# Kernel optimization log

Measured on AMD Instinct MI355X. Metric: run time of the kernel, lower is better.

## Reference

```python
import jax, jax.numpy as jnp
import numpy as np

N_NODES = 100000
N_EDGES = 1600000
IN_CH = 512
MID_CH = 64   # hard-coded mid_layer_channel in the module
OUT_CH = 40


def setup_inputs() -> dict:
    key = jax.random.key(0)
    k0, k1, k2, k3 = jax.random.split(key, 4)
    node_feature = jax.random.normal(k0, (N_NODES, IN_CH), dtype=jnp.float32)
    # edge index [2, E]: row 0 = src, row 1 = dst
    adj_list = jax.random.randint(k1, (2, N_EDGES), 0, N_NODES, dtype=jnp.int32)
    # GCNConv parameters (Glorot-ish scale)
    W1 = jax.random.normal(k2, (IN_CH, MID_CH), dtype=jnp.float32) * (1.0 / np.sqrt(IN_CH))
    b1 = jnp.zeros((MID_CH,), dtype=jnp.float32)
    W2 = jax.random.normal(k3, (MID_CH, OUT_CH), dtype=jnp.float32) * (1.0 / np.sqrt(MID_CH))
    b2 = jnp.zeros((OUT_CH,), dtype=jnp.float32)
    return {"node_feature": node_feature, "adj_list": adj_list,
            "W1": W1, "b1": b1, "W2": W2, "b2": b2}


def _gcn_conv(x, W, b, src, dst, deg_inv_sqrt, n_nodes):
    # Standard GCNConv: D^{-1/2} (A + I) D^{-1/2} (x W) + b
    h = x @ W                                             # [N, F_out]
    norm = deg_inv_sqrt[src] * deg_inv_sqrt[dst]          # [E]
    agg = jax.ops.segment_sum(h[src] * norm[:, None], dst, num_segments=n_nodes)
    agg = agg + h * (deg_inv_sqrt * deg_inv_sqrt)[:, None]  # self-loop term
    return agg + b


def reference(node_feature, adj_list, W1, b1, W2, b2):
    n = node_feature.shape[0]
    src, dst = adj_list[0], adj_list[1]
    # degree with self-loops (in-degree at dst + 1)
    deg = jax.ops.segment_sum(jnp.ones_like(dst, dtype=node_feature.dtype), dst,
                              num_segments=n) + 1.0
    deg_inv_sqrt = jax.lax.rsqrt(deg)
    h = jax.nn.elu(_gcn_conv(node_feature, W1, b1, src, dst, deg_inv_sqrt, n))
    out = _gcn_conv(h, W2, b2, src, dst, deg_inv_sqrt, n)
    return jax.nn.log_softmax(out, axis=1)
```

## Files before the change

### kernel.cpp

```cpp
#include <hip/hip_runtime.h>
#include <hip/hip_bf16.h>
#include <math.h>

#define IN_CH 512
#define MID_CH 64
#define OUT_CH 40

typedef __attribute__((ext_vector_type(8))) short short8;
typedef __attribute__((ext_vector_type(4))) float f32x4;
typedef __attribute__((ext_vector_type(2))) float f32x2;

static __device__ __forceinline__ unsigned short f2bf(float f) {
    unsigned int u = __float_as_uint(f);
    u += 0x7fffu + ((u >> 16) & 1u);
    return (unsigned short)(u >> 16);
}

__global__ void k_count(const int* __restrict__ dst, int* __restrict__ cnt, int E) {
    int pb = blockIdx.x & 7;
    int ch = blockIdx.x >> 3;
    int nch = gridDim.x >> 3;
    int ech = (E + nch - 1) / nch;
    int e0 = ch * ech;
    int e1 = e0 + ech; if (e1 > E) e1 = E;
    for (int e = e0 + threadIdx.x; e < e1; e += blockDim.x) {
        int d = dst[e];
        if ((d & 7) == pb) atomicAdd(&cnt[d], 1);
    }
}

__global__ void k_scanA(const int* __restrict__ cnt, int* __restrict__ rowptr,
                        int* __restrict__ bsum, float* __restrict__ dis, int N) {
    __shared__ int wsum[16];
    int i = blockIdx.x * 1024 + threadIdx.x;
    int lane = threadIdx.x & 63, wv = threadIdx.x >> 6;
    int v = (i < N) ? cnt[i] : 0;
    if (i < N) dis[i] = rsqrtf((float)v + 1.0f);
    int x = (v + 3) & ~3;
    #pragma unroll
    for (int off = 1; off < 64; off <<= 1) {
        int t = __shfl_up(x, off);
        if (lane >= off) x += t;
    }
    if (lane == 63) wsum[wv] = x;
    __syncthreads();
    if (wv == 0 && lane < 16) {
        int own = wsum[lane];
        int y = own;
        #pragma unroll
        for (int off = 1; off < 16; off <<= 1) {
            int t = __shfl_up(y, off);
            if (lane >= off) y += t;
        }
        wsum[lane] = y - own;
        if (lane == 15) bsum[blockIdx.x] = y;
    }
    __syncthreads();
    if (i < N) rowptr[i + 1] = x + wsum[wv];
}

__global__ void k_scanB(int* __restrict__ bsum, int nb) {
    __shared__ int tmp[2];
    int lane = threadIdx.x & 63, wv = threadIdx.x >> 6;
    int v = (threadIdx.x < nb) ? bsum[threadIdx.x] : 0;
    int x = v;
    #pragma unroll
    for (int off = 1; off < 64; off <<= 1) {
        int t = __shfl_up(x, off);
        if (lane >= off) x += t;
    }
    if (lane == 63) tmp[wv] = x;
    __syncthreads();
    int add = (wv == 1) ? tmp[0] : 0;
    if (threadIdx.x < nb) bsum[threadIdx.x] = x - v + add;
}

__global__ void k_scanC(int* __restrict__ rowptr, int* __restrict__ cur,
                        const int* __restrict__ bsum, int N) {
    int i = blockIdx.x * 1024 + threadIdx.x;
    if (i < N) {
        int v = rowptr[i + 1] + bsum[blockIdx.x];
        rowptr[i + 1] = v;
        cur[i + 1] = v;
    }
    if (i == 0) { rowptr[0] = 0; cur[0] = 0; }
}

__global__ void k_padfill(int* __restrict__ esrc, int dummy_off, int total) {
    int i = blockIdx.x * blockDim.x + threadIdx.x;
    if (i < total) esrc[i] = dummy_off;
}

__global__ void k_fill(const int* __restrict__ src, const int* __restrict__ dst,
                       int* __restrict__ cur, int* __restrict__ esrc, int E) {
    int pb = blockIdx.x & 7;
    int ch = blockIdx.x >> 3;
    int nch = gridDim.x >> 3;
    int ech = (E + nch - 1) / nch;
    int e0 = ch * ech;
    int e1 = e0 + ech; if (e1 > E) e1 = E;
    #pragma unroll 4
    for (int e = e0 + (int)threadIdx.x; e < e1; e += blockDim.x) {
        int d = dst[e];
        if ((d & 7) == pb) {
            int p = atomicAdd(&cur[d], 1);
            esrc[p] = src[e] << 6;
        }
    }
}

__global__ void k_prepw(const float* __restrict__ W1, unsigned short* __restrict__ w1f) {
    int f = blockIdx.x * 256 + threadIdx.x;
    int k = f >> 6, c = f & 63;
    w1f[(((k >> 3) * 64) + c) * 8 + (k & 7)] = f2bf(W1[f]);
}

__launch_bounds__(256, 6)
__global__ void k_gemm1(const float* __restrict__ X, const unsigned short* __restrict__ w1f,
                        const float* __restrict__ dis, unsigned char* __restrict__ h1q,
                        int N) {
    int wave = threadIdx.x >> 6, lane = threadIdx.x & 63;
    int rbase = blockIdx.x * 64 + wave * 16;
    int g = lane >> 4;
    int arow = rbase + (lane & 15);
    if (arow > N - 1) arow = N - 1;
    const float* xp = X + (size_t)arow * IN_CH + g * 8;
    const short8* wb = (const short8*)w1f;

    f32x4 acc[4];
    #pragma unroll
    for (int i = 0; i < 4; ++i) acc[i] = (f32x4){0.f, 0.f, 0.f, 0.f};

    float4 bx0[2], bx1[2];
    {
        const float4* p0 = (const float4*)(xp);
        const float4* p1 = (const float4*)(xp + 32);
        bx0[0] = p0[0]; bx1[0] = p0[1];
        bx0[1] = p1[0]; bx1[1] = p1[1];
    }

    #pragma unroll
    for (int ks = 0; ks < 16; ++ks) {
        float4 x0 = bx0[ks & 1], x1 = bx1[ks & 1];
        if (ks < 14) {
            const float4* p = (const float4*)(xp + (ks + 2) * 32);
            bx0[ks & 1] = p[0]; bx1[ks & 1] = p[1];
        }
        short8 a;
        a[0] = (short)f2bf(x0.x); a[1] = (short)f2bf(x0.y);
        a[2] = (short)f2bf(x0.z); a[3] = (short)f2bf(x0.w);
        a[4] = (short)f2bf(x1.x); a[5] = (short)f2bf(x1.y);
        a[6] = (short)f2bf(x1.z); a[7] = (short)f2bf(x1.w);

        int cibase = (ks * 4 + g) * 64 + (lane & 15);
        #pragma unroll
        for (int ct = 0; ct < 4; ++ct) {
            short8 b = wb[cibase + ct * 16];
            acc[ct] = __builtin_amdgcn_mfma_f32_16x16x32_bf16(a, b, acc[ct], 0, 0, 0);
        }
    }

    int colb = lane & 15;
    int rquad = rbase + (lane >> 4) * 4;
    #pragma unroll
    for (int ct = 0; ct < 4; ++ct) {
        #pragma unroll
        for (int r = 0; r < 4; ++r) {
            int row = rquad + r;
            if (row < N) {
                float v = acc[ct][r] * dis[row];
                unsigned q = __builtin_amdgcn_cvt_pk_fp8_f32(v, v, 0, false);
                h1q[(size_t)row * 64 + ct * 16 + colb] = (unsigned char)q;
            }
        }
    }
}

#define AGG_UNPACK8(Q)                                              \
    {                                                               \
        f32x2 lo_ = __builtin_amdgcn_cvt_pk_f32_fp8((Q), false);    \
        f32x2 hi_ = __builtin_amdgcn_cvt_pk_f32_fp8((Q), true);     \
        acc[0] += lo_[0]; acc[1] += lo_[1];                         \
        acc[2] += hi_[0]; acc[3] += hi_[1];                         \
    }

__launch_bounds__(256)
__global__ void k_agg1(const unsigned char* __restrict__ hq, const float* __restrict__ dis,
                       const int* __restrict__ rowptr, const int* __restrict__ esrc,
                       const float* __restrict__ b1, unsigned char* __restrict__ h2q,
                       int N) {
    int wv = threadIdx.x >> 6, lane = threadIdx.x & 63;
    int n = blockIdx.x * 4 + wv;
    if (n >= N) return;
    int g = lane >> 4, cg = lane & 15;
    int beg = rowptr[n], end = rowptr[n + 1];
    unsigned cgoff = (unsigned)(cg * 4);
    const char* hb = (const char*)hq;

    f32x4 acc = (f32x4){0.f, 0.f, 0.f, 0.f};
    for (int cbeg = beg; cbeg < end; cbeg += 64) {
        int m = end - cbeg; if (m > 64) m = 64;
        int soff = esrc[cbeg + lane];
        int k4n = m >> 2;
        int k4 = 0;
        for (; k4 + 4 <= k4n; k4 += 4) {
            int o0 = __shfl(soff, (k4 + 0) * 4 + g);
            int o1 = __shfl(soff, (k4 + 1) * 4 + g);
            int o2 = __shfl(soff, (k4 + 2) * 4 + g);
            int o3 = __shfl(soff, (k4 + 3) * 4 + g);
            unsigned q0 = *(const unsigned*)(hb + ((unsigned)o0 + cgoff));
            unsigned q1 = *(const unsigned*)(hb + ((unsigned)o1 + cgoff));
            unsigned q2 = *(const unsigned*)(hb + ((unsigned)o2 + cgoff));
            unsigned q3 = *(const unsigned*)(hb + ((unsigned)o3 + cgoff));
            AGG_UNPACK8(q0) AGG_UNPACK8(q1) AGG_UNPACK8(q2) AGG_UNPACK8(q3)
        }
        for (; k4 < k4n; ++k4) {
            int o = __shfl(soff, k4 * 4 + g);
            unsigned q = *(const unsigned*)(hb + ((unsigned)o + cgoff));
            AGG_UNPACK8(q)
        }
    }
    #pragma unroll
    for (int off = 32; off >= 16; off >>= 1) {
        acc[0] += __shfl_xor(acc[0], off);
        acc[1] += __shfl_xor(acc[1], off);
        acc[2] += __shfl_xor(acc[2], off);
        acc[3] += __shfl_xor(acc[3], off);
    }
    if (g == 0) {
        float dn = dis[n];
        unsigned qs = *(const unsigned*)(hb + ((unsigned)(n * 64) + cgoff));
        f32x2 slo = __builtin_amdgcn_cvt_pk_f32_fp8(qs, false);
        f32x2 shi = __builtin_amdgcn_cvt_pk_f32_fp8(qs, true);
        float4 b4 = *(const float4*)(b1 + cg * 4);
        float v0 = dn * (acc[0] + slo[0]) + b4.x;
        float v1 = dn * (acc[1] + slo[1]) + b4.y;
        float v2 = dn * (acc[2] + shi[0]) + b4.z;
        float v3 = dn * (acc[3] + shi[1]) + b4.w;
        v0 = v0 > 0.f ? v0 : expm1f(v0);
        v1 = v1 > 0.f ? v1 : expm1f(v1);
        v2 = v2 > 0.f ? v2 : expm1f(v2);
        v3 = v3 > 0.f ? v3 : expm1f(v3);
        unsigned w = __builtin_amdgcn_cvt_pk_fp8_f32(dn * v0, dn * v1, 0, false);
        w = __builtin_amdgcn_cvt_pk_fp8_f32(dn * v2, dn * v3, w, true);
        *(unsigned*)(h2q + (size_t)n * 64 + cg * 4) = w;
    }
}

__launch_bounds__(256)
__global__ void k_agg2(const unsigned char* __restrict__ hq, const float* __restrict__ dis,
                       const int* __restrict__ rowptr, const int* __restrict__ esrc,
                       const float* __restrict__ W2, const float* __restrict__ b2,
                       float* __restrict__ out, int N) {
    __shared__ float w2l[MID_CH * OUT_CH];
    __shared__ float vl[4 * MID_CH];
    for (int f = threadIdx.x; f < MID_CH * OUT_CH; f += 256) w2l[f] = W2[f];
    __syncthreads();

    int wv = threadIdx.x >> 6, lane = threadIdx.x & 63;
    int n = blockIdx.x * 4 + wv;
    if (n >= N) return;
    int g = lane >> 4, cg = lane & 15;
    int beg = rowptr[n], end = rowptr[n + 1];
    unsigned cgoff = (unsigned)(cg * 4);
    const char* hb = (const char*)hq;

    f32x4 acc = (f32x4){0.f, 0.f, 0.f, 0.f};
    for (int cbeg = beg; cbeg < end; cbeg += 64) {
        int m = end - cbeg; if (m > 64) m = 64;
        int soff = esrc[cbeg + lane];
        int k4n = m >> 2;
        int k4 = 0;
        for (; k4 + 4 <= k4n; k4 += 4) {
            int o0 = __shfl(soff, (k4 + 0) * 4 + g);
            int o1 = __shfl(soff, (k4 + 1) * 4 + g);
            int o2 = __shfl(soff, (k4 + 2) * 4 + g);
            int o3 = __shfl(soff, (k4 + 3) * 4 + g);
            unsigned q0 = *(const unsigned*)(hb + ((unsigned)o0 + cgoff));
            unsigned q1 = *(const unsigned*)(hb + ((unsigned)o1 + cgoff));
            unsigned q2 = *(const unsigned*)(hb + ((unsigned)o2 + cgoff));
            unsigned q3 = *(const unsigned*)(hb + ((unsigned)o3 + cgoff));
            AGG_UNPACK8(q0) AGG_UNPACK8(q1) AGG_UNPACK8(q2) AGG_UNPACK8(q3)
        }
        for (; k4 < k4n; ++k4) {
            int o = __shfl(soff, k4 * 4 + g);
            unsigned q = *(const unsigned*)(hb + ((unsigned)o + cgoff));
            AGG_UNPACK8(q)
        }
    }
    #pragma unroll
    for (int off = 32; off >= 16; off >>= 1) {
        acc[0] += __shfl_xor(acc[0], off);
        acc[1] += __shfl_xor(acc[1], off);
        acc[2] += __shfl_xor(acc[2], off);
        acc[3] += __shfl_xor(acc[3], off);
    }
    if (g == 0) {
        float dn = dis[n];
        unsigned qs = *(const unsigned*)(hb + ((unsigned)(n * 64) + cgoff));
        f32x2 slo = __builtin_amdgcn_cvt_pk_f32_fp8(qs, false);
        f32x2 shi = __builtin_amdgcn_cvt_pk_f32_fp8(qs, true);
        float4 v;
        v.x = dn * (acc[0] + slo[0]);
        v.y = dn * (acc[1] + slo[1]);
        v.z = dn * (acc[2] + shi[0]);
        v.w = dn * (acc[3] + shi[1]);
        *(float4*)&vl[wv * 64 + cg * 4] = v;
    }

    float o = (lane < OUT_CH) ? b2[lane] : 0.f;
    const float* vrow = &vl[wv * 64];
    #pragma unroll 8
    for (int c = 0; c < MID_CH; ++c)
        o += vrow[c] * w2l[c * OUT_CH + lane];

    float mx = (lane < OUT_CH) ? o : -1e30f;
    #pragma unroll
    for (int off = 32; off > 0; off >>= 1) mx = fmaxf(mx, __shfl_xor(mx, off));
    float e = (lane < OUT_CH) ? expf(o - mx) : 0.f;
    float ssum = e;
    #pragma unroll
    for (int off = 32; off > 0; off >>= 1) ssum += __shfl_xor(ssum, off);
    if (lane < OUT_CH)
        out[(size_t)n * OUT_CH + lane] = o - mx - logf(ssum);
}

extern "C" void kernel_launch(void* const* d_in, const int* in_sizes, int n_in,
                              void* d_out, int out_size, void* d_ws, size_t ws_size,
                              hipStream_t stream) {
    const float* X  = (const float*)d_in[0];
    const int* adj  = (const int*)d_in[1];
    const float* W1 = (const float*)d_in[2];
    const float* b1 = (const float*)d_in[3];
    const float* W2 = (const float*)d_in[4];
    const float* b2 = (const float*)d_in[5];
    float* out = (float*)d_out;

    int N = in_sizes[0] / IN_CH;
    int E = in_sizes[1] / 2;
    const int* srcp = adj;
    const int* dstp = adj + E;
    int nchunk = (N + 1023) / 1024;
    int epad_max = E + 3 * N + 128;

    char* ws = (char*)d_ws;
    size_t off = 0;
    int*   cnt    = (int*)(ws + off);  off += (size_t)N * sizeof(int);
    int*   cur    = (int*)(ws + off);  off += ((size_t)N + 8) * sizeof(int);
    float* dis    = (float*)(ws + off); off += (size_t)N * sizeof(float);
    int*   rowptr = (int*)(ws + off);  off += ((size_t)N + 8) * sizeof(int);
    int*   bsum   = (int*)(ws + off);  off += 128 * sizeof(int);
    int*   esrc   = (int*)(ws + off);  off += (size_t)epad_max * sizeof(int);
    unsigned short* w1f = (unsigned short*)(ws + off); off += (size_t)IN_CH * MID_CH * sizeof(unsigned short);
    unsigned char* h1q = (unsigned char*)(ws + off); off += (size_t)(N + 4) * MID_CH;
    unsigned char* h2q = (unsigned char*)(ws + off); off += (size_t)(N + 4) * MID_CH;

    hipMemsetAsync(cnt, 0, (size_t)N * sizeof(int), stream);
    k_prepw<<<(IN_CH * MID_CH + 255) / 256, 256, 0, stream>>>(W1, w1f);
    k_count<<<512, 256, 0, stream>>>(dstp, cnt, E);
    k_scanA<<<nchunk, 1024, 0, stream>>>(cnt, rowptr, bsum, dis, N);
    k_scanB<<<1, 128, 0, stream>>>(bsum, nchunk);
    k_scanC<<<nchunk, 1024, 0, stream>>>(rowptr, cur, bsum, N);
    k_padfill<<<(epad_max + 255) / 256, 256, 0, stream>>>(esrc, N << 6, epad_max);
    hipMemsetAsync(h1q + (size_t)N * 64, 0, 64, stream);
    hipMemsetAsync(h2q + (size_t)N * 64, 0, 64, stream);

    k_fill<<<1024, 256, 0, stream>>>(srcp, dstp, cur, esrc, E);
    k_gemm1<<<(N + 63) / 64, 256, 0, stream>>>(X, w1f, dis, h1q, N);
    k_agg1<<<(N + 3) / 4, 256, 0, stream>>>(h1q, dis, rowptr, esrc, b1, h2q, N);
    k_agg2<<<(N + 3) / 4, 256, 0, stream>>>(h2q, dis, rowptr, esrc, W2, b2, out, N);
}
```

Measured before the change: 336.9 us.

## Split fp8 feature tables into 32-channel halves to shrink gather working set

Splits the layer-1 and layer-2 fp8 feature tables into two 32-byte-per-node halves and runs each aggregation twice, one pass per half. Each gather pass then reads from a 3.2MB table that fits better in cache. Edge lists are padded to multiples of 8 so each wave processes 8 edges per step. Layer 2 accumulates partial W2 products in an fp32 buffer between passes. The count kernel is also simplified to one atomic per edge. The cost is twice the edge-index traffic and launches, plus an extra partial-output round trip.

```diff
diff --git a/kernel.cpp b/kernel.cpp
--- a/kernel.cpp
+++ b/kernel.cpp
@@ -17,16 +17,8 @@
 }
 
 __global__ void k_count(const int* __restrict__ dst, int* __restrict__ cnt, int E) {
-    int pb = blockIdx.x & 7;
-    int ch = blockIdx.x >> 3;
-    int nch = gridDim.x >> 3;
-    int ech = (E + nch - 1) / nch;
-    int e0 = ch * ech;
-    int e1 = e0 + ech; if (e1 > E) e1 = E;
-    for (int e = e0 + threadIdx.x; e < e1; e += blockDim.x) {
-        int d = dst[e];
-        if ((d & 7) == pb) atomicAdd(&cnt[d], 1);
-    }
+    int i = blockIdx.x * blockDim.x + threadIdx.x;
+    if (i < E) atomicAdd(&cnt[dst[i]], 1);
 }
 
 __global__ void k_scanA(const int* __restrict__ cnt, int* __restrict__ rowptr,
@@ -36,7 +28,7 @@
     int lane = threadIdx.x & 63, wv = threadIdx.x >> 6;
     int v = (i < N) ? cnt[i] : 0;
     if (i < N) dis[i] = rsqrtf((float)v + 1.0f);
-    int x = (v + 3) & ~3;
+    int x = (v + 7) & ~7;
     #pragma unroll
     for (int off = 1; off < 64; off <<= 1) {
         int t = __shfl_up(x, off);
@@ -104,7 +96,7 @@
         int d = dst[e];
         if ((d & 7) == pb) {
             int p = atomicAdd(&cur[d], 1);
-            esrc[p] = src[e] << 6;
+            esrc[p] = src[e] << 5;
         }
     }
 }
@@ -117,7 +109,8 @@
 
 __launch_bounds__(256, 6)
 __global__ void k_gemm1(const float* __restrict__ X, const unsigned short* __restrict__ w1f,
-                        const float* __restrict__ dis, unsigned char* __restrict__ h1q,
+                        const float* __restrict__ dis,
+                        unsigned char* __restrict__ h1A, unsigned char* __restrict__ h1B,
                         int N) {
     int wave = threadIdx.x >> 6, lane = threadIdx.x & 63;
     int rbase = blockIdx.x * 64 + wave * 16;
@@ -164,13 +157,15 @@
     int rquad = rbase + (lane >> 4) * 4;
     #pragma unroll
     for (int ct = 0; ct < 4; ++ct) {
+        unsigned char* tbl = (ct < 2) ? h1A : h1B;
+        int coloff = (ct & 1) * 16 + colb;
         #pragma unroll
         for (int r = 0; r < 4; ++r) {
             int row = rquad + r;
             if (row < N) {
                 float v = acc[ct][r] * dis[row];
                 unsigned q = __builtin_amdgcn_cvt_pk_fp8_f32(v, v, 0, false);
-                h1q[(size_t)row * 64 + ct * 16 + colb] = (unsigned char)q;
+                tbl[(size_t)row * 32 + coloff] = (unsigned char)q;
             }
         }
     }
@@ -184,55 +179,55 @@
         acc[2] += hi_[0]; acc[3] += hi_[1];                         \
     }
 
+#define GATHER_CORE(HB)                                                 \
+    f32x4 acc = (f32x4){0.f, 0.f, 0.f, 0.f};                            \
+    for (int cbeg = beg; cbeg < end; cbeg += 64) {                      \
+        int m = end - cbeg; if (m > 64) m = 64;      \
+        int soff = esrc[cbeg + lane];                                   \
+        int k8n = m >> 3;                                               \
+        int k8 = 0;                                                     \
+        for (; k8 + 2 <= k8n; k8 += 2) {                                \
+            int o0 = __shfl(soff, (k8 + 0) * 8 + g);                    \
+            int o1 = __shfl(soff, (k8 + 1) * 8 + g);                    \
+            unsigned q0 = *(const unsigned*)((HB) + ((unsigned)o0 + cgoff)); \
+            unsigned q1 = *(const unsigned*)((HB) + ((unsigned)o1 + cgoff)); \
+            AGG_UNPACK8(q0) AGG_UNPACK8(q1)                             \
+        }                                                               \
+        for (; k8 < k8n; ++k8) {                                        \
+            int o = __shfl(soff, k8 * 8 + g);                           \
+            unsigned q = *(const unsigned*)((HB) + ((unsigned)o + cgoff)); \
+            AGG_UNPACK8(q)                                              \
+        }                                                               \
+    }                                                                   \
+    _Pragma("unroll")                                                   \
+    for (int off = 32; off >= 8; off >>= 1) {                           \
+        acc[0] += __shfl_xor(acc[0], off);                              \
+        acc[1] += __shfl_xor(acc[1], off);                              \
+        acc[2] += __shfl_xor(acc[2], off);                              \
+        acc[3] += __shfl_xor(acc[3], off);                              \
+    }
+
 __launch_bounds__(256)
 __global__ void k_agg1(const unsigned char* __restrict__ hq, const float* __restrict__ dis,
                        const int* __restrict__ rowptr, const int* __restrict__ esrc,
-                       const float* __restrict__ b1, unsigned char* __restrict__ h2q,
+                       const float* __restrict__ bias, unsigned char* __restrict__ hdst,
                        int N) {
     int wv = threadIdx.x >> 6, lane = threadIdx.x & 63;
     int n = blockIdx.x * 4 + wv;
     if (n >= N) return;
-    int g = lane >> 4, cg = lane & 15;
+    int g = lane >> 3, cg = lane & 7;
     int beg = rowptr[n], end = rowptr[n + 1];
     unsigned cgoff = (unsigned)(cg * 4);
     const char* hb = (const char*)hq;
 
-    f32x4 acc = (f32x4){0.f, 0.f, 0.f, 0.f};
-    for (int cbeg = beg; cbeg < end; cbeg += 64) {
-        int m = end - cbeg; if (m > 64) m = 64;
-        int soff = esrc[cbeg + lane];
-        int k4n = m >> 2;
-        int k4 = 0;
-        for (; k4 + 4 <= k4n; k4 += 4) {
-            int o0 = __shfl(soff, (k4 + 0) * 4 + g);
-            int o1 = __shfl(soff, (k4 + 1) * 4 + g);
-            int o2 = __shfl(soff, (k4 + 2) * 4 + g);
-            int o3 = __shfl(soff, (k4 + 3) * 4 + g);
-            unsigned q0 = *(const unsigned*)(hb + ((unsigned)o0 + cgoff));
-            unsigned q1 = *(const unsigned*)(hb + ((unsigned)o1 + cgoff));
-            unsigned q2 = *(const unsigned*)(hb + ((unsigned)o2 + cgoff));
-            unsigned q3 = *(const unsigned*)(hb + ((unsigned)o3 + cgoff));
-            AGG_UNPACK8(q0) AGG_UNPACK8(q1) AGG_UNPACK8(q2) AGG_UNPACK8(q3)
-        }
-        for (; k4 < k4n; ++k4) {
-            int o = __shfl(soff, k4 * 4 + g);
-            unsigned q = *(const unsigned*)(hb + ((unsigned)o + cgoff));
-            AGG_UNPACK8(q)
-        }
-    }
-    #pragma unroll
-    for (int off = 32; off >= 16; off >>= 1) {
-        acc[0] += __shfl_xor(acc[0], off);
-        acc[1] += __shfl_xor(acc[1], off);
-        acc[2] += __shfl_xor(acc[2], off);
-        acc[3] += __shfl_xor(acc[3], off);
-    }
+    GATHER_CORE(hb)
+
     if (g == 0) {
         float dn = dis[n];
-        unsigned qs = *(const unsigned*)(hb + ((unsigned)(n * 64) + cgoff));
+        unsigned qs = *(const unsigned*)(hb + ((unsigned)(n * 32) + cgoff));
         f32x2 slo = __builtin_amdgcn_cvt_pk_f32_fp8(qs, false);
         f32x2 shi = __builtin_amdgcn_cvt_pk_f32_fp8(qs, true);
-        float4 b4 = *(const float4*)(b1 + cg * 4);
+        float4 b4 = *(const float4*)(bias + cg * 4);
         float v0 = dn * (acc[0] + slo[0]) + b4.x;
         float v1 = dn * (acc[1] + slo[1]) + b4.y;
         float v2 = dn * (acc[2] + shi[0]) + b4.z;
@@ -243,61 +238,34 @@
         v3 = v3 > 0.f ? v3 : expm1f(v3);
         unsigned w = __builtin_amdgcn_cvt_pk_fp8_f32(dn * v0, dn * v1, 0, false);
         w = __builtin_amdgcn_cvt_pk_fp8_f32(dn * v2, dn * v3, w, true);
-        *(unsigned*)(h2q + (size_t)n * 64 + cg * 4) = w;
+        *(unsigned*)(hdst + (size_t)n * 32 + cg * 4) = w;
     }
 }
 
 __launch_bounds__(256)
 __global__ void k_agg2(const unsigned char* __restrict__ hq, const float* __restrict__ dis,
                        const int* __restrict__ rowptr, const int* __restrict__ esrc,
-                       const float* __restrict__ W2, const float* __restrict__ b2,
-                       float* __restrict__ out, int N) {
-    __shared__ float w2l[MID_CH * OUT_CH];
-    __shared__ float vl[4 * MID_CH];
-    for (int f = threadIdx.x; f < MID_CH * OUT_CH; f += 256) w2l[f] = W2[f];
+                       const float* __restrict__ W2half, const float* __restrict__ b2,
+                       float* __restrict__ opart, float* __restrict__ out,
+                       int N, int final_pass) {
+    __shared__ float w2l[32 * OUT_CH + 64];
+    __shared__ float vl[4 * 32];
+    for (int f = threadIdx.x; f < 32 * OUT_CH; f += 256) w2l[f] = W2half[f];
     __syncthreads();
 
     int wv = threadIdx.x >> 6, lane = threadIdx.x & 63;
     int n = blockIdx.x * 4 + wv;
     if (n >= N) return;
-    int g = lane >> 4, cg = lane & 15;
+    int g = lane >> 3, cg = lane & 7;
     int beg = rowptr[n], end = rowptr[n + 1];
     unsigned cgoff = (unsigned)(cg * 4);
     const char* hb = (const char*)hq;
 
-    f32x4 acc = (f32x4){0.f, 0.f, 0.f, 0.f};
-    for (int cbeg = beg; cbeg < end; cbeg += 64) {
-        int m = end - cbeg; if (m > 64) m = 64;
-        int soff = esrc[cbeg + lane];
-        int k4n = m >> 2;
-        int k4 = 0;
-        for (; k4 + 4 <= k4n; k4 += 4) {
-            int o0 = __shfl(soff, (k4 + 0) * 4 + g);
-            int o1 = __shfl(soff, (k4 + 1) * 4 + g);
-            int o2 = __shfl(soff, (k4 + 2) * 4 + g);
-            int o3 = __shfl(soff, (k4 + 3) * 4 + g);
-            unsigned q0 = *(const unsigned*)(hb + ((unsigned)o0 + cgoff));
-            unsigned q1 = *(const unsigned*)(hb + ((unsigned)o1 + cgoff));
-            unsigned q2 = *(const unsigned*)(hb + ((unsigned)o2 + cgoff));
-            unsigned q3 = *(const unsigned*)(hb + ((unsigned)o3 + cgoff));
-            AGG_UNPACK8(q0) AGG_UNPACK8(q1) AGG_UNPACK8(q2) AGG_UNPACK8(q3)
-        }
-        for (; k4 < k4n; ++k4) {
-            int o = __shfl(soff, k4 * 4 + g);
-            unsigned q = *(const unsigned*)(hb + ((unsigned)o + cgoff));
-            AGG_UNPACK8(q)
-        }
-    }
-    #pragma unroll
-    for (int off = 32; off >= 16; off >>= 1) {
-        acc[0] += __shfl_xor(acc[0], off);
-        acc[1] += __shfl_xor(acc[1], off);
-        acc[2] += __shfl_xor(acc[2], off);
-        acc[3] += __shfl_xor(acc[3], off);
-    }
+    GATHER_CORE(hb)
+
     if (g == 0) {
         float dn = dis[n];
-        unsigned qs = *(const unsigned*)(hb + ((unsigned)(n * 64) + cgoff));
+        unsigned qs = *(const unsigned*)(hb + ((unsigned)(n * 32) + cgoff));
         f32x2 slo = __builtin_amdgcn_cvt_pk_f32_fp8(qs, false);
         f32x2 shi = __builtin_amdgcn_cvt_pk_f32_fp8(qs, true);
         float4 v;
@@ -305,15 +273,21 @@
         v.y = dn * (acc[1] + slo[1]);
         v.z = dn * (acc[2] + shi[0]);
         v.w = dn * (acc[3] + shi[1]);
-        *(float4*)&vl[wv * 64 + cg * 4] = v;
-    }
-
-    float o = (lane < OUT_CH) ? b2[lane] : 0.f;
-    const float* vrow = &vl[wv * 64];
+        *(float4*)&vl[wv * 32 + cg * 4] = v;
+    }
+
+    float o;
+    if (final_pass) o = (lane < OUT_CH) ? opart[(size_t)n * OUT_CH + lane] : 0.f;
+    else            o = (lane < OUT_CH) ? b2[lane] : 0.f;
+    const float* vrow = &vl[wv * 32];
     #pragma unroll 8
-    for (int c = 0; c < MID_CH; ++c)
+    for (int c = 0; c < 32; ++c)
         o += vrow[c] * w2l[c * OUT_CH + lane];
 
+    if (!final_pass) {
+        if (lane < OUT_CH) opart[(size_t)n * OUT_CH + lane] = o;
+        return;
+    }
     float mx = (lane < OUT_CH) ? o : -1e30f;
     #pragma unroll
     for (int off = 32; off > 0; off >>= 1) mx = fmaxf(mx, __shfl_xor(mx, off));
@@ -341,7 +315,7 @@
     const int* srcp = adj;
     const int* dstp = adj + E;
     int nchunk = (N + 1023) / 1024;
-    int epad_max = E + 3 * N + 128;
+    int epad_max = E + 7 * N + 128;
 
     char* ws = (char*)d_ws;
     size_t off = 0;
@@ -352,21 +326,30 @@
     int*   bsum   = (int*)(ws + off);  off += 128 * sizeof(int);
     int*   esrc   = (int*)(ws + off);  off += (size_t)epad_max * sizeof(int);
     unsigned short* w1f = (unsigned short*)(ws + off); off += (size_t)IN_CH * MID_CH * sizeof(unsigned short);
-    unsigned char* h1q = (unsigned char*)(ws + off); off += (size_t)(N + 4) * MID_CH;
-    unsigned char* h2q = (unsigned char*)(ws + off); off += (size_t)(N + 4) * MID_CH;
+    unsigned char* h1A = (unsigned char*)(ws + off); off += (size_t)(N + 4) * 32;
+    unsigned char* h1B = (unsigned char*)(ws + off); off += (size_t)(N + 4) * 32;
+    unsigned char* h2A = (unsigned char*)(ws + off); off += (size_t)(N + 4) * 32;
+    unsigned char* h2B = (unsigned char*)(ws + off); off += (size_t)(N + 4) * 32;
+    float* opart = (float*)(ws + off); off += (size_t)N * OUT_CH * sizeof(float);
 
     hipMemsetAsync(cnt, 0, (size_t)N * sizeof(int), stream);
     k_prepw<<<(IN_CH * MID_CH + 255) / 256, 256, 0, stream>>>(W1, w1f);
-    k_count<<<512, 256, 0, stream>>>(dstp, cnt, E);
+    k_count<<<(E + 255) / 256, 256, 0, stream>>>(dstp, cnt, E);
     k_scanA<<<nchunk, 1024, 0, stream>>>(cnt, rowptr, bsum, dis, N);
     k_scanB<<<1, 128, 0, stream>>>(bsum, nchunk);
     k_scanC<<<nchunk, 1024, 0, stream>>>(rowptr, cur, bsum, N);
-    k_padfill<<<(epad_max + 255) / 256, 256, 0, stream>>>(esrc, N << 6, epad_max);
-    hipMemsetAsync(h1q + (size_t)N * 64, 0, 64, stream);
-    hipMemsetAsync(h2q + (size_t)N * 64, 0, 64, stream);
+    k_padfill<<<(epad_max + 255) / 256, 256, 0, stream>>>(esrc, N << 5, epad_max);
+    hipMemsetAsync(h1A + (size_t)N * 32, 0, 32, stream);
+    hipMemsetAsync(h1B + (size_t)N * 32, 0, 32, stream);
+    hipMemsetAsync(h2A + (size_t)N * 32, 0, 32, stream);
+    hipMemsetAsync(h2B + (size_t)N * 32, 0, 32, stream);
 
     k_fill<<<1024, 256, 0, stream>>>(srcp, dstp, cur, esrc, E);
-    k_gemm1<<<(N + 63) / 64, 256, 0, stream>>>(X, w1f, dis, h1q, N);
-    k_agg1<<<(N + 3) / 4, 256, 0, stream>>>(h1q, dis, rowptr, esrc, b1, h2q, N);
-    k_agg2<<<(N + 3) / 4, 256, 0, stream>>>(h2q, dis, rowptr, esrc, W2, b2, out, N);
-}
+    k_gemm1<<<(N + 63) / 64, 256, 0, stream>>>(X, w1f, dis, h1A, h1B, N);
+
+    int nb = (N + 3) / 4;
+    k_agg1<<<nb, 256, 0, stream>>>(h1A, dis, rowptr, esrc, b1,      h2A, N);
+    k_agg1<<<nb, 256, 0, stream>>>(h1B, dis, rowptr, esrc, b1 + 32, h2B, N);
+    k_agg2<<<nb, 256, 0, stream>>>(h2A, dis, rowptr, esrc, W2,           b2, opart, out, N, 0);
+    k_agg2<<<nb, 256, 0, stream>>>(h2B, dis, rowptr, esrc, W2 + 32 * OUT_CH, b2, opart, out, N, 1);
+}
```

Measured after the change: 406.0 us. +20.5%, slower.
